# Kernel optimization log

Measured on AMD Instinct MI355X. Metric: run time of the kernel, lower is better.

The kernel has to match this reference:

```python
import jax, jax.numpy as jnp
import numpy as np

N, E, D, H, C = 100000, 1600000, 128, 256, 40


def setup_inputs() -> dict:
    key = jax.random.key(0)
    ks = jax.random.split(key, 10)
    x = jax.random.normal(ks[0], (N, D), dtype=jnp.float32)
    src = jax.random.randint(ks[1], (E,), 0, N, dtype=jnp.int32)
    dst = jax.random.randint(ks[2], (E,), 0, N, dtype=jnp.int32)
    # GIN layer 1 MLP (bias-free), kaiming-uniform-like scale 1/sqrt(fan_in)
    w1a = jax.random.normal(ks[3], (D, H), dtype=jnp.float32) / np.sqrt(D)
    w1b = jax.random.normal(ks[4], (H, H), dtype=jnp.float32) / np.sqrt(H)
    # GIN layer 2 MLP
    w2a = jax.random.normal(ks[5], (H, H), dtype=jnp.float32) / np.sqrt(H)
    w2b = jax.random.normal(ks[6], (H, H), dtype=jnp.float32) / np.sqrt(H)
    # eps initialized to 0 per reset_parameters
    eps1 = jnp.zeros((), dtype=jnp.float32)
    eps2 = jnp.zeros((), dtype=jnp.float32)
    # final classifier fc (with bias)
    fc_w = jax.random.normal(ks[7], (H, C), dtype=jnp.float32) / np.sqrt(H)
    fc_b = jax.random.normal(ks[8], (C,), dtype=jnp.float32) * 0.01
    return {"x": x, "src": src, "dst": dst,
            "eps1": eps1, "w1a": w1a, "w1b": w1b,
            "eps2": eps2, "w2a": w2a, "w2b": w2b,
            "fc_w": fc_w, "fc_b": fc_b}


def reference(x, src, dst, eps1, w1a, w1b, eps2, w2a, w2b, fc_w, fc_b):
    n = x.shape[0]

    def gin_layer(h, eps, wa, wb):
        # GINConv sum-aggregation: scatter-add neighbor feats over edges
        agg = jax.ops.segment_sum(h[src], dst, num_segments=n)  # [N, d]
        rst = (1.0 + eps) * h + agg
        # 2-layer bias-free MLP with ReLU between
        return jax.nn.relu(rst @ wa) @ wb

    h = jax.nn.relu(gin_layer(x, eps1, w1a, w1b))   # layer + outer activation
    h = jax.nn.relu(gin_layer(h, eps2, w2a, w2b))   # dropout p=0 -> identity
    return h @ fc_w + fc_b                           # [N, C]
```

## Files before the change

### kernel.cpp

```cpp
#include <hip/hip_runtime.h>

#define N_NODES 100000
#define NPAD    100032
#define N_EDGES 1600000
#define DIM_IN  128
#define DIM_H   256
#define DIM_C   40

#define NB   391
#define NBLK 391
#define CHUNK 4096
#define ECAP 6144

#define CVT_BLOCKS 25000
#define WCVT_BLOCKS 1280

typedef unsigned short bf16_t;
typedef __attribute__((ext_vector_type(8))) short short8;
typedef __attribute__((ext_vector_type(4))) float f32x4;

__device__ __forceinline__ bf16_t f2b(float f) {
    unsigned int u = __float_as_uint(f);
    unsigned int r = (u + 0x7fffu + ((u >> 16) & 1u)) >> 16;
    return (bf16_t)r;
}

__device__ __forceinline__ void gl_lds16(const void* gsrc, void* ldst) {
    __builtin_amdgcn_global_load_lds(
        (const __attribute__((address_space(1))) void*)gsrc,
        (__attribute__((address_space(3))) void*)ldst,
        16, 0, 0);
}


__global__ __launch_bounds__(256) void k_prep(
    const int* __restrict__ dst, int* __restrict__ cnt2,
    const float* __restrict__ x, signed char* __restrict__ x8, float* __restrict__ xs,
    const float* __restrict__ w1a, const float* __restrict__ w1b,
    const float* __restrict__ w2a, const float* __restrict__ w2b,
    const float* __restrict__ fcw,
    bf16_t* __restrict__ o1a, bf16_t* __restrict__ o1b,
    bf16_t* __restrict__ o2a, bf16_t* __restrict__ o2b, bf16_t* __restrict__ ofc,
    int* __restrict__ ticket)
{
    __shared__ int h[NB];
    int blk = blockIdx.x, t = threadIdx.x;

    if (blk < NBLK) {
        if (blk == 0 && t == 0) *ticket = 0;
        for (int i = t; i < NB; i += 256) h[i] = 0;
        __syncthreads();
        int base = blk * CHUNK;
        int end = min(base + CHUNK, N_EDGES);
        for (int i = base + t; i < end; i += 256)
            atomicAdd(&h[dst[i] >> 8], 1);
        __syncthreads();
        for (int i = t; i < NB; i += 256) cnt2[blk * NB + i] = h[i];
        return;
    }
    blk -= NBLK;

    if (blk < CVT_BLOCKS) {
        int gid = blk * 256 + t;
        int u = gid >> 6, lane = gid & 63;
        float2 v = *(const float2*)(x + (size_t)u * 128 + lane * 2);
        float m = fmaxf(fabsf(v.x), fabsf(v.y));
        #pragma unroll
        for (int d = 1; d < 64; d <<= 1)
            m = fmaxf(m, __shfl_xor(m, d, 64));
        float inv = (m > 0.f) ? 127.f / m : 0.f;
        int q0 = (int)rintf(v.x * inv);
        int q1 = (int)rintf(v.y * inv);
        unsigned short pk = (unsigned short)((q0 & 0xff) | ((q1 & 0xff) << 8));
        *(unsigned short*)(x8 + ((unsigned)u << 7) + lane * 2) = pk;
        if (lane == 0) xs[u] = (m > 0.f) ? m * (1.f / 127.f) : 0.f;
        return;
    }
    blk -= CVT_BLOCKS;

    int r = blk >> 8;
    int idx = (blk & 255) * 256 + t;
    const float* in; bf16_t* out; int K, N, Npad;
    switch (r) {
        case 0: in = w1a; out = o1a; K = 128; N = 256; Npad = 256; break;
        case 1: in = w1b; out = o1b; K = 256; N = 256; Npad = 256; break;
        case 2: in = w2a; out = o2a; K = 256; N = 256; Npad = 256; break;
        case 3: in = w2b; out = o2b; K = 256; N = 256; Npad = 256; break;
        default: in = fcw; out = ofc; K = 256; N = 40;  Npad = 64;  break;
    }
    if (idx >= Npad * K) return;
    int n = idx / K, k = idx - n * K;
    float v = (n < N) ? in[(size_t)k * N + n] : 0.f;
    int kstep = k >> 5, quad = (k >> 3) & 3, e = k & 7;
    int tt = n >> 4, l15 = n & 15;
    size_t opos = (size_t)kstep * (Npad * 32) + ((size_t)(tt * 64 + quad * 16 + l15)) * 8 + e;
    out[opos] = f2b(v);
}


__global__ void k_bscanA(const int* __restrict__ cnt2, int* __restrict__ basep,
                         int* __restrict__ btot, int* __restrict__ ticket,
                         int* __restrict__ boff) {
    __shared__ int s[512];
    __shared__ int isLast;
    int t = threadIdx.x, b = blockIdx.x;
    int v = (t < NBLK) ? cnt2[t * NB + b] : 0;
    s[t] = v;
    __syncthreads();
    #pragma unroll
    for (int d = 1; d < 512; d <<= 1) {
        int tv = (t >= d) ? s[t - d] : 0;
        __syncthreads();
        s[t] += tv;
        __syncthreads();
    }
    if (t < NBLK) basep[t * NB + b] = s[t] - v;
    if (t == 511) atomicExch(&btot[b], s[511]);
    __syncthreads();
    if (t == 0) {
        __threadfence();
        int old = atomicAdd(ticket, 1);
        isLast = (old == NB - 1);
    }
    __syncthreads();
    if (!isLast) return;

    __threadfence();
    int v2 = (t < NB) ? atomicAdd(&btot[t], 0) : 0;
    s[t] = v2;
    __syncthreads();
    #pragma unroll
    for (int d = 1; d < 512; d <<= 1) {
        int tv = (t >= d) ? s[t - d] : 0;
        __syncthreads();
        s[t] += tv;
        __syncthreads();
    }
    if (t < NB) boff[t] = s[t] - v2;
    if (t == NB - 1) boff[NB] = s[t];
}

__global__ void k_bscatter(const int* __restrict__ src, const int* __restrict__ dst,
                           const int* __restrict__ basep, const int* __restrict__ boff,
                           int* __restrict__ ebuf, int e) {
    __shared__ int cur[NB];
    int t = threadIdx.x, blk = blockIdx.x;
    for (int i = t; i < NB; i += 256) cur[i] = basep[blk * NB + i] + boff[i];
    __syncthreads();
    int base = blk * CHUNK;
    int end = min(base + CHUNK, e);
    for (int i = base + t; i < end; i += 256) {
        int sv = src[i], dv = dst[i];
        int pos = atomicAdd(&cur[dv >> 8], 1);
        ebuf[pos] = sv | ((dv & 255) << 24);
    }
}

__global__ __launch_bounds__(256) void k_build(const int* __restrict__ ebuf,
                                               const int* __restrict__ boff,
                                               int* __restrict__ off,
                                               int* __restrict__ csr) {
    __shared__ int ec[ECAP];
    __shared__ int h[256];
    __shared__ int cur[256];
    int t = threadIdx.x, b = blockIdx.x;
    int node0 = b << 8;
    int e0 = boff[b], e1 = boff[b + 1];
    int ne = e1 - e0;
    bool fits = (ne <= ECAP);
    h[t] = 0;
    __syncthreads();
    if (fits) {
        for (int i = t; i < ne; i += 256) {
            int p = ebuf[e0 + i];
            ec[i] = p;
            atomicAdd(&h[(unsigned)p >> 24], 1);
        }
    } else {
        for (int i = t; i < ne; i += 256)
            atomicAdd(&h[(unsigned)ebuf[e0 + i] >> 24], 1);
    }
    __syncthreads();
    int mydeg = h[t];
    #pragma unroll
    for (int d = 1; d < 256; d <<= 1) {
        int tv = (t >= d) ? h[t - d] : 0;
        __syncthreads();
        h[t] += tv;
        __syncthreads();
    }
    int node = node0 + t;
    if (node < N_NODES) off[node + 1] = e0 + h[t];
    if (b == 0 && t == 0) off[0] = 0;
    cur[t] = e0 + h[t] - mydeg;
    __syncthreads();
    if (fits) {
        for (int i = t; i < ne; i += 256) {
            int p = ec[i];
            int pos = atomicAdd(&cur[(unsigned)p >> 24], 1);
            csr[pos] = p & 0xFFFFFF;
        }
    } else {
        for (int i = t; i < ne; i += 256) {
            int p = ebuf[e0 + i];
            int pos = atomicAdd(&cur[(unsigned)p >> 24], 1);
            csr[pos] = p & 0xFFFFFF;
        }
    }
}


__global__ void k_agg_i8(const signed char* __restrict__ h8, const float* __restrict__ hs,
                         const int* __restrict__ off, const int* __restrict__ csr,
                         const float* __restrict__ eps_p,
                         bf16_t* __restrict__ rst, int n) {
    int gid = blockIdx.x * blockDim.x + threadIdx.x;
    int u = __builtin_amdgcn_readfirstlane(gid >> 6);
    int lane = threadIdx.x & 63;
    if (u >= n) return;

    float acc0 = 0.f, acc1 = 0.f;
    int r0 = off[u], r1 = off[u + 1];
    unsigned loff = lane * 2u;

    for (int base = r0; base < r1; base += 64) {
        int m = r1 - base; if (m > 64) m = 64;
        int li = (lane < m) ? lane : (m - 1);
        int iv = csr[base + li];
        for (int c = 0; c < m; c += 16) {
            int s[16]; float sc[16]; unsigned v[16];
            #pragma unroll
            for (int t = 0; t < 16; t++)
                s[t] = __builtin_amdgcn_readlane(iv, c + t);
            #pragma unroll
            for (int t = 0; t < 16; t++)
                sc[t] = (c + t < m) ? hs[s[t]] : 0.f;
            #pragma unroll
            for (int t = 0; t < 16; t++)
                v[t] = *(const unsigned short*)(h8 + (((unsigned)s[t] << 7) + loff));
            #pragma unroll
            for (int t = 0; t < 16; t++) {
                acc0 += (float)(int)(signed char)(v[t] & 0xffu) * sc[t];
                acc1 += (float)(int)(signed char)(v[t] >> 8) * sc[t];
            }
        }
    }

    float scu = hs[u] * (1.0f + eps_p[0]);
    unsigned vu = *(const unsigned short*)(h8 + (((unsigned)u << 7) + loff));
    float o0 = (float)(int)(signed char)(vu & 0xffu) * scu + acc0;
    float o1 = (float)(int)(signed char)(vu >> 8) * scu + acc1;

    int R = u >> 6, rr = u & 63;
    int i4 = rr >> 4, l15v = rr & 15;
    int ks = lane >> 4, quad = (lane >> 2) & 3, e2 = (lane & 3) * 2;
    size_t pos = (((size_t)R * 4 + ks) * 256 + (size_t)(i4 * 64 + quad * 16 + l15v)) * 8 + e2;
    *(unsigned int*)(rst + pos) =
        (unsigned int)f2b(o0) | ((unsigned int)f2b(o1) << 16);
}


__global__ void k_agg_u8(const unsigned char* __restrict__ h8,
                         const float* __restrict__ hs,
                         const int* __restrict__ off, const int* __restrict__ csr,
                         const float* __restrict__ eps_p,
                         bf16_t* __restrict__ rst, int n) {
    int gid = blockIdx.x * blockDim.x + threadIdx.x;
    int u = __builtin_amdgcn_readfirstlane(gid >> 6);
    int lane = threadIdx.x & 63;
    if (u >= n) return;

    float acc[4] = {0.f, 0.f, 0.f, 0.f};
    int r0 = off[u], r1 = off[u + 1];
    unsigned loff = lane * 4u;

    for (int base = r0; base < r1; base += 64) {
        int m = r1 - base; if (m > 64) m = 64;
        int li = (lane < m) ? lane : (m - 1);
        int iv = csr[base + li];
        for (int c = 0; c < m; c += 16) {
            int s[16]; float sc[16]; unsigned int v[16];
            #pragma unroll
            for (int t = 0; t < 16; t++)
                s[t] = __builtin_amdgcn_readlane(iv, c + t);
            #pragma unroll
            for (int t = 0; t < 16; t++)
                sc[t] = (c + t < m) ? hs[s[t]] : 0.f;
            #pragma unroll
            for (int t = 0; t < 16; t++)
                v[t] = *(const unsigned int*)(h8 + (((unsigned)s[t] << 8) + loff));
            #pragma unroll
            for (int t = 0; t < 16; t++) {
                acc[0] += (float)(v[t] & 0xffu) * sc[t];
                acc[1] += (float)((v[t] >> 8) & 0xffu) * sc[t];
                acc[2] += (float)((v[t] >> 16) & 0xffu) * sc[t];
                acc[3] += (float)(v[t] >> 24) * sc[t];
            }
        }
    }

    float ep = 1.0f + eps_p[0];
    unsigned int vu = *(const unsigned int*)(h8 + (((unsigned)u << 8) + loff));
    float scu = hs[u] * ep;
    float o0 = (float)(vu & 0xffu) * scu + acc[0];
    float o1 = (float)((vu >> 8) & 0xffu) * scu + acc[1];
    float o2 = (float)((vu >> 16) & 0xffu) * scu + acc[2];
    float o3 = (float)(vu >> 24) * scu + acc[3];
    uint2 ov;
    ov.x = (unsigned int)f2b(o0) | ((unsigned int)f2b(o1) << 16);
    ov.y = (unsigned int)f2b(o2) | ((unsigned int)f2b(o3) << 16);

    int R = u >> 6, rr = u & 63;
    int i4 = rr >> 4, l15v = rr & 15;
    int ks = lane >> 3, quad = (lane >> 1) & 3, e4 = (lane & 1) * 4;
    size_t pos = (((size_t)R * 8 + ks) * 256 + (size_t)(i4 * 64 + quad * 16 + l15v)) * 8 + e4;
    *(uint2*)(rst + pos) = ov;
}


template <int K1, bool OUT8, bool FUSE_FC>
__global__ __launch_bounds__(512, 4) void k_mlp(
    const bf16_t* __restrict__ A, const bf16_t* __restrict__ W1t,
    const bf16_t* __restrict__ W2t, bf16_t* __restrict__ H,
    unsigned char* __restrict__ H8, float* __restrict__ Hs,
    const bf16_t* __restrict__ FCt, const float* __restrict__ fc_b,
    float* __restrict__ Cout, int M)
{
    constexpr int NS1 = K1 / 32;
    __shared__ __align__(16) bf16_t As[2][64 * 32];
    __shared__ __align__(16) bf16_t Bs[2][256 * 32];
    __shared__ __align__(16) bf16_t Ts[64 * 256];
    __shared__ int rmax[64];

    int tid = threadIdx.x;
    int wave = tid >> 6, lane = tid & 63;
    int l15 = lane & 15, quad = lane >> 4;
    int bm = blockIdx.x * 64;
    int wn = wave * 32;

    auto stageA = [&](int kstep, int b) {
        if (tid < 256)
            gl_lds16(A + ((size_t)blockIdx.x * NS1 + kstep) * 2048 + tid * 8, &As[b][tid * 8]);
    };
    auto stageB = [&](const bf16_t* W, int kstep, int b) {
        #pragma unroll
        for (int l = 0; l < 2; l++) {
            int c = l * 512 + tid;
            gl_lds16(W + ((size_t)kstep * 1024 + c) * 8, &Bs[b][c * 8]);
        }
    };

    auto ts_el = [&](int row, int col) {
        return ((col >> 5) * 4 + (row >> 4)) * 512 +
               ((((col >> 3) & 3) * 16) + (row & 15)) * 8 + (col & 7);
    };

    f32x4 acc[4][2];
    #pragma unroll
    for (int i = 0; i < 4; i++)
        #pragma unroll
        for (int j = 0; j < 2; j++) acc[i][j] = 0.f;

    stageA(0, 0); stageB(W1t, 0, 0);
    #pragma unroll
    for (int k = 0; k < NS1; k++) {
        int cur = k & 1;
        if (k + 1 < NS1) {
            stageA(k + 1, cur ^ 1); stageB(W1t, k + 1, cur ^ 1);
            if (tid < 256) { asm volatile("s_waitcnt vmcnt(3)" ::: "memory"); }
            else           { asm volatile("s_waitcnt vmcnt(2)" ::: "memory"); }
        } else {
            asm volatile("s_waitcnt vmcnt(0)" ::: "memory");
        }
        __builtin_amdgcn_sched_barrier(0);
        __builtin_amdgcn_s_barrier();

        short8 af[4], bfv[2];
        #pragma unroll
        for (int i = 0; i < 4; i++)
            af[i] = *(const short8*)&As[cur][(i * 64 + lane) * 8];
        #pragma unroll
        for (int j = 0; j < 2; j++)
            bfv[j] = *(const short8*)&Bs[cur][((wave * 2 + j) * 64 + lane) * 8];

        #pragma unroll
        for (int i = 0; i < 4; i++)
            #pragma unroll
            for (int j = 0; j < 2; j++)
                acc[i][j] = __builtin_amdgcn_mfma_f32_16x16x32_bf16(af[i], bfv[j], acc[i][j], 0, 0, 0);

        asm volatile("s_waitcnt lgkmcnt(0)" ::: "memory");
        __builtin_amdgcn_sched_barrier(0);
        __builtin_amdgcn_s_barrier();
    }

    #pragma unroll
    for (int i = 0; i < 4; i++)
        #pragma unroll
        for (int j = 0; j < 2; j++) {
            int col = wn + j * 16 + l15;
            #pragma unroll
            for (int r = 0; r < 4; r++) {
                int row = i * 16 + quad * 4 + r;
                Ts[ts_el(row, col)] = f2b(fmaxf(acc[i][j][r], 0.f));
            }
        }

    #pragma unroll
    for (int i = 0; i < 4; i++)
        #pragma unroll
        for (int j = 0; j < 2; j++) acc[i][j] = 0.f;
    __syncthreads();

    stageB(W2t, 0, 0);
    #pragma unroll
    for (int k = 0; k < 8; k++) {
        int cur = k & 1;
        if (k + 1 < 8) {
            stageB(W2t, k + 1, cur ^ 1);
            asm volatile("s_waitcnt vmcnt(2)" ::: "memory");
        } else {
            asm volatile("s_waitcnt vmcnt(0)" ::: "memory");
        }
        __builtin_amdgcn_sched_barrier(0);
        __builtin_amdgcn_s_barrier();

        short8 af[4], bfv[2];
        #pragma unroll
        for (int i = 0; i < 4; i++)
            af[i] = *(const short8*)&Ts[((k * 4 + i) * 64 + lane) * 8];
        #pragma unroll
        for (int j = 0; j < 2; j++)
            bfv[j] = *(const short8*)&Bs[cur][((wave * 2 + j) * 64 + lane) * 8];

        #pragma unroll
        for (int i = 0; i < 4; i++)
            #pragma unroll
            for (int j = 0; j < 2; j++)
                acc[i][j] = __builtin_amdgcn_mfma_f32_16x16x32_bf16(af[i], bfv[j], acc[i][j], 0, 0, 0);

        asm volatile("s_waitcnt lgkmcnt(0)" ::: "memory");
        __builtin_amdgcn_sched_barrier(0);
        __builtin_amdgcn_s_barrier();
    }

    if constexpr (OUT8) {
        if (tid < 64) rmax[tid] = 0;
        __syncthreads();
        #pragma unroll
        for (int i = 0; i < 4; i++)
            #pragma unroll
            for (int r = 0; r < 4; r++) {
                float m = 0.f;
                #pragma unroll
                for (int j = 0; j < 2; j++) m = fmaxf(m, acc[i][j][r]);
                atomicMax(&rmax[i * 16 + quad * 4 + r], __float_as_int(m));
            }
        __syncthreads();
        #pragma unroll
        for (int i = 0; i < 4; i++) {
            #pragma unroll
            for (int r = 0; r < 4; r++) {
                int row = i * 16 + quad * 4 + r;
                int rowg = bm + row;
                if (rowg >= M) continue;
                float rm = __int_as_float(rmax[row]);
                float inv = (rm > 0.f) ? 255.f / rm : 0.f;
                #pragma unroll
                for (int j = 0; j < 2; j++) {
                    int col = wn + j * 16 + l15;
                    float v = fmaxf(acc[i][j][r], 0.f);
                    unsigned q = (unsigned)(v * inv + 0.5f);
                    if (q > 255u) q = 255u;
                    H8[(size_t)rowg * 256 + col] = (unsigned char)q;
                }
                if (wave == 0 && l15 == 0)
                    Hs[rowg] = rm * (1.f / 255.f);
            }
        }
    } else if constexpr (FUSE_FC) {
        #pragma unroll
        for (int i = 0; i < 4; i++)
            #pragma unroll
            for (int j = 0; j < 2; j++) {
                int col = wn + j * 16 + l15;
                #pragma unroll
                for (int r = 0; r < 4; r++) {
                    int row = i * 16 + quad * 4 + r;
                    Ts[ts_el(row, col)] = f2b(fmaxf(acc[i][j][r], 0.f));
                }
            }
        __syncthreads();

        f32x4 acc3[3];
        #pragma unroll
        for (int j = 0; j < 3; j++) acc3[j] = 0.f;

        auto stage3 = [&](int kstep, int b) {
            if (tid < 256)
                gl_lds16(FCt + ((size_t)kstep * 256 + tid) * 8, &Bs[b][tid * 8]);
        };

        stage3(0, 0);
        #pragma unroll
        for (int k = 0; k < 8; k++) {
            int cur = k & 1;
            if (k + 1 < 8) {
                stage3(k + 1, cur ^ 1);
                if (tid < 256) { asm volatile("s_waitcnt vmcnt(1)" ::: "memory"); }
            } else {
                if (tid < 256) { asm volatile("s_waitcnt vmcnt(0)" ::: "memory"); }
            }
            __builtin_amdgcn_sched_barrier(0);
            __builtin_amdgcn_s_barrier();

            if (tid < 256) {
                short8 af = *(const short8*)&Ts[((k * 4 + wave) * 64 + lane) * 8];
                #pragma unroll
                for (int j = 0; j < 3; j++) {
                    short8 bfv = *(const short8*)&Bs[cur][((j * 64) + lane) * 8];
                    acc3[j] = __builtin_amdgcn_mfma_f32_16x16x32_bf16(af, bfv, acc3[j], 0, 0, 0);
                }
                asm volatile("s_waitcnt lgkmcnt(0)" ::: "memory");
            }
            __builtin_amdgcn_sched_barrier(0);
            __builtin_amdgcn_s_barrier();
        }

        if (tid < 256) {
            #pragma unroll
            for (int j = 0; j < 3; j++) {
                int col = j * 16 + l15;
                if (col >= DIM_C) continue;
                float bv = fc_b[col];
                #pragma unroll
                for (int r = 0; r < 4; r++) {
                    int rowg = bm + wave * 16 + quad * 4 + r;
                    if (rowg < M)
                        Cout[(size_t)rowg * DIM_C + col] = acc3[j][r] + bv;
                }
            }
        }
    } else {
        #pragma unroll
        for (int j = 0; j < 2; j++) {
            int col = wn + j * 16 + l15;
            #pragma unroll
            for (int i = 0; i < 4; i++) {
                #pragma unroll
                for (int r = 0; r < 4; r++) {
                    int rowg = bm + i * 16 + quad * 4 + r;
                    if (rowg < M)
                        H[(size_t)rowg * 256 + col] = f2b(fmaxf(acc[i][j][r], 0.f));
                }
            }
        }
    }
}


static inline size_t rnd256(size_t x) { return (x + 255) & ~(size_t)255; }

extern "C" void kernel_launch(void* const* d_in, const int* in_sizes, int n_in,
                              void* d_out, int out_size, void* d_ws, size_t ws_size,
                              hipStream_t stream) {
    const float* x    = (const float*)d_in[0];
    const int*   src  = (const int*)d_in[1];
    const int*   dst  = (const int*)d_in[2];
    const float* eps1 = (const float*)d_in[3];
    const float* w1a  = (const float*)d_in[4];
    const float* w1b  = (const float*)d_in[5];
    const float* eps2 = (const float*)d_in[6];
    const float* w2a  = (const float*)d_in[7];
    const float* w2b  = (const float*)d_in[8];
    const float* fc_w = (const float*)d_in[9];
    const float* fc_b = (const float*)d_in[10];
    float* out = (float*)d_out;

    char* w = (char*)d_ws;
    int* off  = (int*)w; w += rnd256(sizeof(int) * (size_t)(N_NODES + 1));
    int* csr  = (int*)w; w += rnd256(sizeof(int) * (size_t)N_EDGES);
    int* cnt2  = (int*)w; w += rnd256(sizeof(int) * (size_t)NBLK * NB);
    int* basep = (int*)w; w += rnd256(sizeof(int) * (size_t)NBLK * NB);
    int* btot  = (int*)w; w += rnd256(sizeof(int) * 512);
    int* boff  = (int*)w; w += rnd256(sizeof(int) * (NB + 1));
    bf16_t* w1a_t = (bf16_t*)w; w += rnd256(2 * (size_t)DIM_H * DIM_IN);
    bf16_t* w1b_t = (bf16_t*)w; w += rnd256(2 * (size_t)DIM_H * DIM_H);
    bf16_t* w2a_t = (bf16_t*)w; w += rnd256(2 * (size_t)DIM_H * DIM_H);
    bf16_t* w2b_t = (bf16_t*)w; w += rnd256(2 * (size_t)DIM_H * DIM_H);
    bf16_t* fc_t  = (bf16_t*)w; w += rnd256(2 * (size_t)128 * DIM_H);
    signed char* x8 = (signed char*)w; w += rnd256((size_t)N_NODES * DIM_IN);
    float* xs = (float*)w; w += rnd256(sizeof(float) * (size_t)N_NODES);
    unsigned char* h8 = (unsigned char*)w; w += rnd256((size_t)N_NODES * DIM_H);
    float* hs = (float*)w; w += rnd256(sizeof(float) * (size_t)N_NODES);
    bf16_t* R12 = (bf16_t*)w; w += rnd256(2 * (size_t)NPAD * DIM_H);
    bf16_t* R3  = (bf16_t*)w; w += rnd256(2 * (size_t)NPAD * DIM_H);

    bf16_t* rst1 = R12;
    int* ebuf = (int*)R3;
    int* ticket = btot + 500;

    k_prep<<<NBLK + CVT_BLOCKS + WCVT_BLOCKS, 256, 0, stream>>>(
        dst, cnt2, x, x8, xs, w1a, w1b, w2a, w2b, fc_w,
        w1a_t, w1b_t, w2a_t, w2b_t, fc_t, ticket);

    k_bscanA<<<NB, 512, 0, stream>>>(cnt2, basep, btot, ticket, boff);
    k_bscatter<<<NBLK, 256, 0, stream>>>(src, dst, basep, boff, ebuf, N_EDGES);
    k_build<<<NB, 256, 0, stream>>>(ebuf, boff, off, csr);

    const int agg_blocks = (N_NODES * 64 + 255) / 256;
    const int mlp_blocks = NPAD / 64;

    k_agg_i8<<<agg_blocks, 256, 0, stream>>>(x8, xs, off, csr, eps1, rst1, N_NODES);
    k_mlp<DIM_IN, true, false><<<mlp_blocks, 512, 0, stream>>>(
        rst1, w1a_t, w1b_t, nullptr, h8, hs, nullptr, nullptr, nullptr, N_NODES);

    k_agg_u8<<<agg_blocks, 256, 0, stream>>>(h8, hs, off, csr, eps2, (bf16_t*)R3, N_NODES);
    k_mlp<DIM_H, false, true><<<mlp_blocks, 512, 0, stream>>>(
        (bf16_t*)R3, w2a_t, w2b_t, nullptr, nullptr, nullptr, fc_t, fc_b, out, N_NODES);
}
```

Before: 413.3 us.

## Single-buffer MLP LDS staging to raise occupancy to six blocks per CU

Result: no change. 408.8 us (-1.1%).

```diff
diff --git a/kernel.cpp b/kernel.cpp
--- a/kernel.cpp
+++ b/kernel.cpp
@@ -319,7 +319,7 @@
 
 
 template <int K1, bool OUT8, bool FUSE_FC>
-__global__ __launch_bounds__(512, 4) void k_mlp(
+__global__ __launch_bounds__(512, 6) void k_mlp(
     const bf16_t* __restrict__ A, const bf16_t* __restrict__ W1t,
     const bf16_t* __restrict__ W2t, bf16_t* __restrict__ H,
     unsigned char* __restrict__ H8, float* __restrict__ Hs,
@@ -327,8 +327,8 @@
     float* __restrict__ Cout, int M)
 {
     constexpr int NS1 = K1 / 32;
-    __shared__ __align__(16) bf16_t As[2][64 * 32];
-    __shared__ __align__(16) bf16_t Bs[2][256 * 32];
+    __shared__ __align__(16) bf16_t As[64 * 32];
+    __shared__ __align__(16) bf16_t Bs[256 * 32];
     __shared__ __align__(16) bf16_t Ts[64 * 256];
     __shared__ int rmax[64];
 
@@ -338,15 +338,15 @@
     int bm = blockIdx.x * 64;
     int wn = wave * 32;
 
-    auto stageA = [&](int kstep, int b) {
+    auto stageA = [&](int kstep) {
         if (tid < 256)
-            gl_lds16(A + ((size_t)blockIdx.x * NS1 + kstep) * 2048 + tid * 8, &As[b][tid * 8]);
+            gl_lds16(A + ((size_t)blockIdx.x * NS1 + kstep) * 2048 + tid * 8, &As[tid * 8]);
     };
-    auto stageB = [&](const bf16_t* W, int kstep, int b) {
+    auto stageB = [&](const bf16_t* W, int kstep) {
         #pragma unroll
         for (int l = 0; l < 2; l++) {
             int c = l * 512 + tid;
-            gl_lds16(W + ((size_t)kstep * 1024 + c) * 8, &Bs[b][c * 8]);
+            gl_lds16(W + ((size_t)kstep * 1024 + c) * 8, &Bs[c * 8]);
         }
     };
 
@@ -361,27 +361,20 @@
         #pragma unroll
         for (int j = 0; j < 2; j++) acc[i][j] = 0.f;
 
-    stageA(0, 0); stageB(W1t, 0, 0);
     #pragma unroll
     for (int k = 0; k < NS1; k++) {
-        int cur = k & 1;
-        if (k + 1 < NS1) {
-            stageA(k + 1, cur ^ 1); stageB(W1t, k + 1, cur ^ 1);
-            if (tid < 256) { asm volatile("s_waitcnt vmcnt(3)" ::: "memory"); }
-            else           { asm volatile("s_waitcnt vmcnt(2)" ::: "memory"); }
-        } else {
-            asm volatile("s_waitcnt vmcnt(0)" ::: "memory");
-        }
+        stageA(k); stageB(W1t, k);
+        asm volatile("s_waitcnt vmcnt(0)" ::: "memory");
         __builtin_amdgcn_sched_barrier(0);
         __builtin_amdgcn_s_barrier();
 
         short8 af[4], bfv[2];
         #pragma unroll
         for (int i = 0; i < 4; i++)
-            af[i] = *(const short8*)&As[cur][(i * 64 + lane) * 8];
+            af[i] = *(const short8*)&As[(i * 64 + lane) * 8];
         #pragma unroll
         for (int j = 0; j < 2; j++)
-            bfv[j] = *(const short8*)&Bs[cur][((wave * 2 + j) * 64 + lane) * 8];
+            bfv[j] = *(const short8*)&Bs[((wave * 2 + j) * 64 + lane) * 8];
 
         #pragma unroll
         for (int i = 0; i < 4; i++)
@@ -389,8 +382,6 @@
             for (int j = 0; j < 2; j++)
                 acc[i][j] = __builtin_amdgcn_mfma_f32_16x16x32_bf16(af[i], bfv[j], acc[i][j], 0, 0, 0);
 
-        asm volatile("s_waitcnt lgkmcnt(0)" ::: "memory");
-        __builtin_amdgcn_sched_barrier(0);
         __builtin_amdgcn_s_barrier();
     }
 
@@ -412,16 +403,10 @@
         for (int j = 0; j < 2; j++) acc[i][j] = 0.f;
     __syncthreads();
 
-    stageB(W2t, 0, 0);
     #pragma unroll
     for (int k = 0; k < 8; k++) {
-        int cur = k & 1;
-        if (k + 1 < 8) {
-            stageB(W2t, k + 1, cur ^ 1);
-            asm volatile("s_waitcnt vmcnt(2)" ::: "memory");
-        } else {
-            asm volatile("s_waitcnt vmcnt(0)" ::: "memory");
-        }
+        stageB(W2t, k);
+        asm volatile("s_waitcnt vmcnt(0)" ::: "memory");
         __builtin_amdgcn_sched_barrier(0);
         __builtin_amdgcn_s_barrier();
 
@@ -431,7 +416,7 @@
             af[i] = *(const short8*)&Ts[((k * 4 + i) * 64 + lane) * 8];
         #pragma unroll
         for (int j = 0; j < 2; j++)
-            bfv[j] = *(const short8*)&Bs[cur][((wave * 2 + j) * 64 + lane) * 8];
+            bfv[j] = *(const short8*)&Bs[((wave * 2 + j) * 64 + lane) * 8];
 
         #pragma unroll
         for (int i = 0; i < 4; i++)
@@ -439,8 +424,6 @@
             for (int j = 0; j < 2; j++)
                 acc[i][j] = __builtin_amdgcn_mfma_f32_16x16x32_bf16(af[i], bfv[j], acc[i][j], 0, 0, 0);
 
-        asm volatile("s_waitcnt lgkmcnt(0)" ::: "memory");
-        __builtin_amdgcn_sched_barrier(0);
         __builtin_amdgcn_s_barrier();
     }
 
@@ -496,34 +479,29 @@
         #pragma unroll
         for (int j = 0; j < 3; j++) acc3[j] = 0.f;
 
-        auto stage3 = [&](int kstep, int b) {
-            if (tid < 256)
-                gl_lds16(FCt + ((size_t)kstep * 256 + tid) * 8, &Bs[b][tid * 8]);
-        };
-
-        stage3(0, 0);
-        #pragma unroll
-        for (int k = 0; k < 8; k++) {
-            int cur = k & 1;
-            if (k + 1 < 8) {
-                stage3(k + 1, cur ^ 1);
-                if (tid < 256) { asm volatile("s_waitcnt vmcnt(1)" ::: "memory"); }
-            } else {
-                if (tid < 256) { asm volatile("s_waitcnt vmcnt(0)" ::: "memory"); }
-            }
+        #pragma unroll
+        for (int hh = 0; hh < 2; hh++) {
+            #pragma unroll
+            for (int l = 0; l < 2; l++) {
+                int c = l * 512 + tid;
+                gl_lds16(FCt + ((size_t)hh * 1024 + c) * 8, &Bs[c * 8]);
+            }
+            asm volatile("s_waitcnt vmcnt(0)" ::: "memory");
             __builtin_amdgcn_sched_barrier(0);
             __builtin_amdgcn_s_barrier();
 
             if (tid < 256) {
-                short8 af = *(const short8*)&Ts[((k * 4 + wave) * 64 + lane) * 8];
                 #pragma unroll
-                for (int j = 0; j < 3; j++) {
-                    short8 bfv = *(const short8*)&Bs[cur][((j * 64) + lane) * 8];
-                    acc3[j] = __builtin_amdgcn_mfma_f32_16x16x32_bf16(af, bfv, acc3[j], 0, 0, 0);
+                for (int kk = 0; kk < 4; kk++) {
+                    int k = hh * 4 + kk;
+                    short8 af = *(const short8*)&Ts[((k * 4 + wave) * 64 + lane) * 8];
+                    #pragma unroll
+                    for (int j = 0; j < 3; j++) {
+                        short8 bfv = *(const short8*)&Bs[((kk * 256) + j * 64 + lane) * 8];
+                        acc3[j] = __builtin_amdgcn_mfma_f32_16x16x32_bf16(af, bfv, acc3[j], 0, 0, 0);
+                    }
                 }
-                asm volatile("s_waitcnt lgkmcnt(0)" ::: "memory");
-            }
-            __builtin_amdgcn_sched_barrier(0);
+            }
             __builtin_amdgcn_s_barrier();
         }
 
```
